# Kernel optimization log

Hardware: AMD Instinct MI355X
Metric: run time of the kernel (lower is better)

## Reference

```python
import jax, jax.numpy as jnp
import numpy as np

N_NODES = 100000
N_EDGES = 1600000
K = 3


def _cheb_conv(x, row, col, w, W, b):
    # SpMM: out[row] += w * x[col]
    def spmm(v):
        return jax.ops.segment_sum(w[:, None] * v[col], row, num_segments=N_NODES)
    Ts = [x, spmm(x)]
    for _ in range(2, K):
        Ts.append(2.0 * spmm(Ts[-1]) - Ts[-2])
    return jnp.concatenate(Ts, axis=-1) @ W.T + b


def setup_inputs() -> dict:
    key = jax.random.key(0)
    ks = jax.random.split(key, 12)
    inp = {
        "x": jax.random.normal(ks[0], (N_NODES, 128), dtype=jnp.float32),
        "edge_index": jax.random.randint(ks[1], (2, N_EDGES), 0, N_NODES, dtype=jnp.int32),
        "edge_weight": jax.random.normal(ks[2], (N_EDGES,), dtype=jnp.float32) * 0.05,
        "W_in": jax.random.normal(ks[3], (128, K * 128), dtype=jnp.float32) * (1.0 / np.sqrt(K * 128)),
        "b_in": jnp.zeros((128,), dtype=jnp.float32),
        "W_h1": jax.random.normal(ks[4], (128, K * 128), dtype=jnp.float32) * (1.0 / np.sqrt(K * 128)),
        "b_h1": jnp.zeros((128,), dtype=jnp.float32),
        "W_h2": jax.random.normal(ks[5], (128, K * 128), dtype=jnp.float32) * (1.0 / np.sqrt(K * 128)),
        "b_h2": jnp.zeros((128,), dtype=jnp.float32),
        "W_out": jax.random.normal(ks[6], (64, K * 128), dtype=jnp.float32) * (1.0 / np.sqrt(K * 128)),
        "b_out": jnp.zeros((64,), dtype=jnp.float32),
    }
    return inp


def reference(x, edge_index, edge_weight, W_in, b_in, W_h1, b_h1, W_h2, b_h2, W_out, b_out):
    row, col = edge_index[0], edge_index[1]
    # dropout is inactive at inference (training=False)
    h = jax.nn.relu(_cheb_conv(x, row, col, edge_weight, W_in, b_in))
    for (W, b) in ((W_h1, b_h1), (W_h2, b_h2)):
        h = jax.nn.relu(_cheb_conv(h, row, col, edge_weight, W, b) + h)  # residual
    out = _cheb_conv(h, row, col, edge_weight, W_out, b_out)
    return out
```

## Files before the change

kernel.cpp:

```cpp
#include <hip/hip_runtime.h>
#include <hip/hip_bf16.h>
#include <stdint.h>
#include <stddef.h>

#define N_NODES 100000
#define N_EDGES 1600000
#define FEAT 128
#define NB_SCAN ((N_NODES + 255) / 256)
#define LDS_PITCH 136
#define CAP 24
#define NL (CAP / 4)

typedef __attribute__((ext_vector_type(8))) short bf16x8;
typedef __attribute__((ext_vector_type(4))) float f32x4;
typedef unsigned short u16;

__device__ __forceinline__ float bf2f(u16 u) {
    union { unsigned int i; float f; } v; v.i = ((unsigned int)u) << 16; return v.f;
}
__device__ __forceinline__ u16 f2bf(float f) {
    union { float f; unsigned int i; } v; v.f = f;
    unsigned int x = v.i;
    return (u16)((x + 0x7fffu + ((x >> 16) & 1u)) >> 16);
}


__global__ void hist_kernel(const int* __restrict__ rows, int* __restrict__ counts) {
    int e = blockIdx.x * blockDim.x + threadIdx.x;
    if (e < N_EDGES) {
        int r = rows[e];
        r = min(max(r, 0), N_NODES - 1);
        atomicAdd(&counts[r], 1);
    }
}

__global__ void reduce_counts_kernel(const int* __restrict__ counts, int* __restrict__ bsum) {
    __shared__ int s[256];
    int i = blockIdx.x * 256 + threadIdx.x;
    int v = (i < N_NODES) ? counts[i] : 0;
    s[threadIdx.x] = v; __syncthreads();
    for (int off = 128; off > 0; off >>= 1) {
        if (threadIdx.x < off) s[threadIdx.x] += s[threadIdx.x + off];
        __syncthreads();
    }
    if (threadIdx.x == 0) bsum[blockIdx.x] = s[0];
}

__global__ void scan_bsums_kernel(int* __restrict__ bsum, int* __restrict__ row_ptr) {
    __shared__ int s[512];
    int t = threadIdx.x;
    int v = (t < NB_SCAN) ? bsum[t] : 0;
    s[t] = v; __syncthreads();
    for (int off = 1; off < 512; off <<= 1) {
        int x = (t >= off) ? s[t - off] : 0;
        __syncthreads();
        s[t] += x;
        __syncthreads();
    }
    if (t < NB_SCAN) bsum[t] = s[t] - v;
    if (t == NB_SCAN - 1) row_ptr[N_NODES] = s[t];
}

__global__ void write_rowptr_kernel(int* __restrict__ counts, const int* __restrict__ bsum,
                                    int* __restrict__ row_ptr) {
    __shared__ int s[256];
    int i = blockIdx.x * 256 + threadIdx.x;
    int v = (i < N_NODES) ? counts[i] : 0;
    s[threadIdx.x] = v; __syncthreads();
    for (int off = 1; off < 256; off <<= 1) {
        int x = (threadIdx.x >= off) ? s[threadIdx.x - off] : 0;
        __syncthreads();
        s[threadIdx.x] += x;
        __syncthreads();
    }
    if (i < N_NODES) {
        row_ptr[i] = bsum[blockIdx.x] + s[threadIdx.x] - v;
        counts[i] = 0;
    }
}

__global__ void scatter_kernel(const int* __restrict__ rows, const int* __restrict__ cols,
                               const float* __restrict__ w, const int* __restrict__ row_ptr,
                               int* __restrict__ fill, int2* __restrict__ ecw) {
    int e = blockIdx.x * blockDim.x + threadIdx.x;
    if (e < N_EDGES) {
        int r = rows[e];
        r = min(max(r, 0), N_NODES - 1);
        int pos = row_ptr[r] + atomicAdd(&fill[r], 1);
        pos = min(max(pos, 0), N_EDGES - 1);
        int c = cols[e];
        c = min(max(c, 0), N_NODES - 1);
        ecw[pos] = make_int2(c, __float_as_int(w[e]));
    }
}

__device__ __forceinline__ float w_fold(const float* W, int o, int k) {
    if (k < 128)      return W[o * 384 + k] - W[o * 384 + 256 + k];
    else if (k < 256) return W[o * 384 + k];
    else              return 2.0f * W[o * 384 + k];
}

__global__ void prep_w_kernel(const float* __restrict__ W, u16* __restrict__ Wp, int O) {
    int i = blockIdx.x * blockDim.x + threadIdx.x;
    if (i >= O * 384) return;
    int o = i / 384, k = i % 384;
    Wp[i] = f2bf(w_fold(W, o, k));
}

__global__ void prep_w2_kernel(const float* __restrict__ W, u16* __restrict__ Wp2, int O) {
    int i = blockIdx.x * blockDim.x + threadIdx.x;
    int total = (O / 16) * 12 * 64;
    if (i >= total) return;
    int ot = i / 768;
    int rem = i % 768;
    int kk = rem / 64;
    int l = rem % 64;
    int q = l >> 4, r = l & 15;
    int o = ot * 16 + r;
    int kbase = kk * 32 + q * 8;
#pragma unroll
    for (int j = 0; j < 8; ++j)
        Wp2[(size_t)i * 8 + j] = f2bf(w_fold(W, o, kbase + j));
}


__global__ void cvt_kernel(const float* __restrict__ x, u16* __restrict__ y) {
    int i = blockIdx.x * blockDim.x + threadIdx.x;
    if (i >= N_NODES * FEAT / 4) return;
    float4 v = ((const float4*)x)[i];
    ushort4 o;
    o.x = f2bf(v.x); o.y = f2bf(v.y); o.z = f2bf(v.z); o.w = f2bf(v.w);
    ((ushort4*)y)[i] = o;
}


__device__ __forceinline__ void load_meta(const int2* __restrict__ ecw, int s, int n,
                                          int lane, int& call, float& wall) {
    int idx = s + max(0, min(lane, n - 1));
    idx = min(idx, N_EDGES - 1);
    int2 cw = ecw[idx];
    call = cw.x;
    wall = (lane < n) ? __int_as_float(cw.y) : 0.f;
}

__device__ __forceinline__ void issue_row(const u16* __restrict__ X, int call,
                                          int g, int f, bf16x8* q) {
#pragma unroll
    for (int k = 0; k < NL; ++k) {
        int col = __shfl(call, k * 4 + g);
        q[k] = *(const bf16x8*)(X + (size_t)col * FEAT + f * 8);
    }
}

__device__ __forceinline__ void reduce_row(const bf16x8* q, float wall,
                                           int g, float* acc) {
#pragma unroll
    for (int k = 0; k < NL; ++k) {
        float wj = __shfl(wall, k * 4 + g);
#pragma unroll
        for (int j = 0; j < 8; ++j) acc[j] += wj * bf2f((u16)q[k][j]);
    }
}

__device__ __forceinline__ void gather4(const int* __restrict__ row_ptr,
                                        const int2* __restrict__ ecw,
                                        const u16* __restrict__ X,
                                        int r0, int lane, int g, int f,
                                        float acc[4][8]) {
    int s[4], e[4];
    int call[4]; float wall[4];
#pragma unroll
    for (int y = 0; y < 4; ++y) {
        s[y] = row_ptr[r0 + y];
        e[y] = row_ptr[r0 + y + 1];
    }
#pragma unroll
    for (int y = 0; y < 4; ++y)
        load_meta(ecw, s[y], min(e[y] - s[y], CAP), lane, call[y], wall[y]);
#pragma unroll
    for (int y = 0; y < 4; ++y)
#pragma unroll
        for (int j = 0; j < 8; ++j) acc[y][j] = 0.f;

    bf16x8 q0[NL], q1[NL], q2[NL], q3[NL];
    issue_row(X, call[0], g, f, q0);
    issue_row(X, call[1], g, f, q1);
    reduce_row(q0, wall[0], g, acc[0]);
    issue_row(X, call[2], g, f, q2);
    reduce_row(q1, wall[1], g, acc[1]);
    issue_row(X, call[3], g, f, q3);
    reduce_row(q2, wall[2], g, acc[2]);
    reduce_row(q3, wall[3], g, acc[3]);

#pragma unroll
    for (int y = 0; y < 4; ++y) {
        for (int cs = s[y] + CAP; cs < e[y]; cs += CAP) {
            int c2; float w2;
            load_meta(ecw, cs, min(e[y] - cs, CAP), lane, c2, w2);
            bf16x8 qt[NL];
            issue_row(X, c2, g, f, qt);
            reduce_row(qt, w2, g, acc[y]);
        }
    }

#pragma unroll
    for (int y = 0; y < 4; ++y)
#pragma unroll
        for (int j = 0; j < 8; ++j) {
            acc[y][j] += __shfl_xor(acc[y][j], 16);
            acc[y][j] += __shfl_xor(acc[y][j], 32);
        }
}


__global__ __launch_bounds__(256) void spmm_kernel(const int* __restrict__ row_ptr,
                                                   const int2* __restrict__ ecw,
                                                   const u16* __restrict__ X,
                                                   u16* __restrict__ Y) {
    int wid = threadIdx.x >> 6;
    int lane = threadIdx.x & 63;
    int g = lane >> 4, f = lane & 15;
    int r0 = blockIdx.x * 16 + wid * 4;

    float acc[4][8];
    gather4(row_ptr, ecw, X, r0, lane, g, f, acc);

    if (g == 0) {
#pragma unroll
        for (int y = 0; y < 4; ++y) {
            u16 tmp[8];
#pragma unroll
            for (int j = 0; j < 8; ++j) tmp[j] = f2bf(acc[y][j]);
            *(bf16x8*)(Y + (size_t)(r0 + y) * FEAT + f * 8) = *(const bf16x8*)tmp;
        }
    }
}


template <int O, bool RELU, bool RES, bool OUT_F32>
__global__ __launch_bounds__(256) void gemm_kernel(const u16* __restrict__ H,
                                                   const u16* __restrict__ T1,
                                                   const u16* __restrict__ S2,
                                                   const u16* __restrict__ Wp2,
                                                   const float* __restrict__ bias,
                                                   void* __restrict__ outv) {
    __shared__ __align__(16) u16 sA[3][32][LDS_PITCH];
    int tid = threadIdx.x;
    int m0 = blockIdx.x * 32;

#pragma unroll
    for (int p = 0; p < 3; ++p) {
        const u16* sp = (p == 0) ? H : (p == 1) ? T1 : S2;
#pragma unroll
        for (int u = 0; u < 2; ++u) {
            int unit = u * 256 + tid;
            int row = unit >> 4, seg = unit & 15;
            *(bf16x8*)&sA[p][row][seg * 8] =
                *(const bf16x8*)(sp + (size_t)(m0 + row) * FEAT + seg * 8);
        }
    }
    __syncthreads();

    int lane = tid & 63, wid = tid >> 6;
    int r = lane & 15, q = lane >> 4;
    constexpr int NW = O / 64;
    f32x4 acc0[NW], acc1[NW];
#pragma unroll
    for (int t = 0; t < NW; ++t) {
        acc0[t] = (f32x4){0.f, 0.f, 0.f, 0.f};
        acc1[t] = (f32x4){0.f, 0.f, 0.f, 0.f};
    }

#pragma unroll
    for (int kk = 0; kk < 12; ++kk) {
        int p = kk >> 2, ko = kk & 3;
        bf16x8 af0 = *(const bf16x8*)&sA[p][r][ko * 32 + q * 8];
        bf16x8 af1 = *(const bf16x8*)&sA[p][16 + r][ko * 32 + q * 8];
#pragma unroll
        for (int t = 0; t < NW; ++t) {
            int ot = wid * NW + t;
            bf16x8 bfr = *(const bf16x8*)(Wp2 + ((size_t)(ot * 12 + kk) * 64 + lane) * 8);
            acc0[t] = __builtin_amdgcn_mfma_f32_16x16x32_bf16(af0, bfr, acc0[t], 0, 0, 0);
            acc1[t] = __builtin_amdgcn_mfma_f32_16x16x32_bf16(af1, bfr, acc1[t], 0, 0, 0);
        }
    }

#pragma unroll
    for (int t = 0; t < NW; ++t) {
        int col = (wid * NW + t) * 16 + r;
        float bv = bias[col];
#pragma unroll
        for (int i = 0; i < 4; ++i) {
            int lrow = q * 4 + i;
            float v0 = acc0[t][i] + bv;
            if (RES)  v0 += bf2f(sA[0][lrow][col]);
            if (RELU) v0 = fmaxf(v0, 0.f);
            float v1 = acc1[t][i] + bv;
            if (RES)  v1 += bf2f(sA[0][16 + lrow][col]);
            if (RELU) v1 = fmaxf(v1, 0.f);
            if (OUT_F32) {
                ((float*)outv)[(size_t)(m0 + lrow) * O + col] = v0;
                ((float*)outv)[(size_t)(m0 + 16 + lrow) * O + col] = v1;
            } else {
                ((u16*)outv)[(size_t)(m0 + lrow) * O + col] = f2bf(v0);
                ((u16*)outv)[(size_t)(m0 + 16 + lrow) * O + col] = f2bf(v1);
            }
        }
    }
}


template <int O, bool RELU, bool RES, bool OUT_F32>
__global__ __launch_bounds__(256) void fused_gemm_kernel(const int* __restrict__ row_ptr,
                                                         const int2* __restrict__ ecw,
                                                         const u16* __restrict__ H,
                                                         const u16* __restrict__ T1,
                                                         const u16* __restrict__ Wp,
                                                         const float* __restrict__ bias,
                                                         void* __restrict__ outv) {
    __shared__ __align__(16) u16 sT[16 * LDS_PITCH];
    int wid = threadIdx.x >> 6;
    int lane = threadIdx.x & 63;
    int g = lane >> 4, f = lane & 15;
    int m0 = blockIdx.x * 16;

    {
        float acc[4][8];
        gather4(row_ptr, ecw, T1, m0 + wid * 4, lane, g, f, acc);
        if (g == 0) {
#pragma unroll
            for (int y = 0; y < 4; ++y) {
                u16 tmp[8];
#pragma unroll
                for (int j = 0; j < 8; ++j) tmp[j] = f2bf(acc[y][j]);
                *(bf16x8*)(sT + (wid * 4 + y) * LDS_PITCH + f * 8) = *(const bf16x8*)tmp;
            }
        }
    }
    __syncthreads();

    int r = f, q = g;
    constexpr int NT = O / 16;
    constexpr int NW = NT / 4;
    f32x4 acc[NW];
#pragma unroll
    for (int t = 0; t < NW; ++t) acc[t] = (f32x4){0.f, 0.f, 0.f, 0.f};

#pragma unroll
    for (int kk = 0; kk < 12; ++kk) {
        bf16x8 af;
        if (kk < 4)
            af = *(const bf16x8*)(H + (size_t)(m0 + r) * FEAT + kk * 32 + q * 8);
        else if (kk < 8)
            af = *(const bf16x8*)(T1 + (size_t)(m0 + r) * FEAT + (kk - 4) * 32 + q * 8);
        else
            af = *(const bf16x8*)(sT + r * LDS_PITCH + (kk - 8) * 32 + q * 8);
#pragma unroll
        for (int t = 0; t < NW; ++t) {
            int ot = wid * NW + t;
            bf16x8 bfr = *(const bf16x8*)(Wp + (size_t)(ot * 16 + r) * 384 + kk * 32 + q * 8);
            acc[t] = __builtin_amdgcn_mfma_f32_16x16x32_bf16(af, bfr, acc[t], 0, 0, 0);
        }
    }

#pragma unroll
    for (int t = 0; t < NW; ++t) {
        int col = (wid * NW + t) * 16 + r;
        float bv = bias[col];
#pragma unroll
        for (int i = 0; i < 4; ++i) {
            int row = m0 + q * 4 + i;
            float v = acc[t][i] + bv;
            if (RES)  v += bf2f(H[(size_t)row * FEAT + col]);
            if (RELU) v = fmaxf(v, 0.f);
            if (OUT_F32) ((float*)outv)[(size_t)row * O + col] = v;
            else         ((u16*)outv)[(size_t)row * O + col] = f2bf(v);
        }
    }
}


static inline size_t align_up(size_t x) { return (x + 255) & ~(size_t)255; }

extern "C" void kernel_launch(void* const* d_in, const int* in_sizes, int n_in,
                              void* d_out, int out_size, void* d_ws, size_t ws_size,
                              hipStream_t stream) {
    const float* x     = (const float*)d_in[0];
    const int*   ei    = (const int*)d_in[1];
    const float* ew    = (const float*)d_in[2];
    const float* W_in  = (const float*)d_in[3];
    const float* b_in  = (const float*)d_in[4];
    const float* W_h1  = (const float*)d_in[5];
    const float* b_h1  = (const float*)d_in[6];
    const float* W_h2  = (const float*)d_in[7];
    const float* b_h2  = (const float*)d_in[8];
    const float* W_out = (const float*)d_in[9];
    const float* b_out = (const float*)d_in[10];

    const int* rows = ei;
    const int* cols = ei + N_EDGES;

    char* w = (char*)d_ws;
    size_t off = 0;
    int* counts = (int*)(w + off);            off = align_up(off + (size_t)N_NODES * 4);
    int* row_ptr= (int*)(w + off);            off = align_up(off + (size_t)(N_NODES + 1) * 4);
    int* bsum   = (int*)(w + off);            off = align_up(off + 512 * 4);
    int2* ecw   = (int2*)(w + off);           off = align_up(off + (size_t)N_EDGES * 8);
    u16* t1     = (u16*)(w + off);            off = align_up(off + (size_t)N_NODES * FEAT * 2);
    u16* h      = (u16*)(w + off);            off = align_up(off + (size_t)N_NODES * FEAT * 2);
    u16* Wp_in  = (u16*)(w + off);            off = align_up(off + (size_t)128 * 384 * 2);
    u16* Wp_h1  = (u16*)(w + off);            off = align_up(off + (size_t)128 * 384 * 2);
    u16* Wp_h2  = (u16*)(w + off);            off = align_up(off + (size_t)128 * 384 * 2);
    u16* Wp_out = (u16*)(w + off);            off = align_up(off + (size_t)64 * 384 * 2);
    u16* s2     = (u16*)(w + off);            size_t off2 = align_up(off + (size_t)N_NODES * FEAT * 2);
    u16* W2_in  = (u16*)(w + off2);           off2 = align_up(off2 + (size_t)128 * 384 * 2);
    u16* W2_h1  = (u16*)(w + off2);           off2 = align_up(off2 + (size_t)128 * 384 * 2);
    u16* W2_h2  = (u16*)(w + off2);           off2 = align_up(off2 + (size_t)128 * 384 * 2);
    u16* W2_out = (u16*)(w + off2);           off2 = align_up(off2 + (size_t)64 * 384 * 2);
    const bool use_split = (ws_size >= off2);

    hipMemsetAsync(counts, 0, (size_t)N_NODES * 4, stream);

    cvt_kernel<<<(N_NODES * FEAT / 4 + 255) / 256, 256, 0, stream>>>(x, h);

    hist_kernel<<<N_EDGES / 256, 256, 0, stream>>>(rows, counts);
    reduce_counts_kernel<<<NB_SCAN, 256, 0, stream>>>(counts, bsum);
    scan_bsums_kernel<<<1, 512, 0, stream>>>(bsum, row_ptr);
    write_rowptr_kernel<<<NB_SCAN, 256, 0, stream>>>(counts, bsum, row_ptr);
    scatter_kernel<<<N_EDGES / 256, 256, 0, stream>>>(rows, cols, ew, row_ptr, counts, ecw);

    const int grid16 = N_NODES / 16;
    const int grid32 = N_NODES / 32;

    if (use_split) {
        prep_w2_kernel<<<(128 * 384 / 8 + 255) / 256, 256, 0, stream>>>(W_in, W2_in, 128);
        prep_w2_kernel<<<(128 * 384 / 8 + 255) / 256, 256, 0, stream>>>(W_h1, W2_h1, 128);
        prep_w2_kernel<<<(128 * 384 / 8 + 255) / 256, 256, 0, stream>>>(W_h2, W2_h2, 128);
        prep_w2_kernel<<<(64 * 384 / 8 + 255) / 256, 256, 0, stream>>>(W_out, W2_out, 64);

        spmm_kernel<<<grid16, 256, 0, stream>>>(row_ptr, ecw, h, t1);
        spmm_kernel<<<grid16, 256, 0, stream>>>(row_ptr, ecw, t1, s2);
        gemm_kernel<128, true, false, false><<<grid32, 256, 0, stream>>>(h, t1, s2, W2_in, b_in, h);
        spmm_kernel<<<grid16, 256, 0, stream>>>(row_ptr, ecw, h, t1);
        spmm_kernel<<<grid16, 256, 0, stream>>>(row_ptr, ecw, t1, s2);
        gemm_kernel<128, true, true, false><<<grid32, 256, 0, stream>>>(h, t1, s2, W2_h1, b_h1, h);
        spmm_kernel<<<grid16, 256, 0, stream>>>(row_ptr, ecw, h, t1);
        spmm_kernel<<<grid16, 256, 0, stream>>>(row_ptr, ecw, t1, s2);
        gemm_kernel<128, true, true, false><<<grid32, 256, 0, stream>>>(h, t1, s2, W2_h2, b_h2, h);
        spmm_kernel<<<grid16, 256, 0, stream>>>(row_ptr, ecw, h, t1);
        spmm_kernel<<<grid16, 256, 0, stream>>>(row_ptr, ecw, t1, s2);
        gemm_kernel<64, false, false, true><<<grid32, 256, 0, stream>>>(h, t1, s2, W2_out, b_out, d_out);
    } else {
        prep_w_kernel<<<(128 * 384 + 255) / 256, 256, 0, stream>>>(W_in, Wp_in, 128);
        prep_w_kernel<<<(128 * 384 + 255) / 256, 256, 0, stream>>>(W_h1, Wp_h1, 128);
        prep_w_kernel<<<(128 * 384 + 255) / 256, 256, 0, stream>>>(W_h2, Wp_h2, 128);
        prep_w_kernel<<<(64 * 384 + 255) / 256, 256, 0, stream>>>(W_out, Wp_out, 64);

        spmm_kernel<<<grid16, 256, 0, stream>>>(row_ptr, ecw, h, t1);
        fused_gemm_kernel<128, true, false, false><<<grid16, 256, 0, stream>>>(
            row_ptr, ecw, h, t1, Wp_in, b_in, h);
        spmm_kernel<<<grid16, 256, 0, stream>>>(row_ptr, ecw, h, t1);
        fused_gemm_kernel<128, true, true, false><<<grid16, 256, 0, stream>>>(
            row_ptr, ecw, h, t1, Wp_h1, b_h1, h);
        spmm_kernel<<<grid16, 256, 0, stream>>>(row_ptr, ecw, h, t1);
        fused_gemm_kernel<128, true, true, false><<<grid16, 256, 0, stream>>>(
            row_ptr, ecw, h, t1, Wp_h2, b_h2, h);
        spmm_kernel<<<grid16, 256, 0, stream>>>(row_ptr, ecw, h, t1);
        fused_gemm_kernel<64, false, false, true><<<grid16, 256, 0, stream>>>(
            row_ptr, ecw, h, t1, Wp_out, b_out, d_out);
    }
}
```

Before: 826.8 us.

## Build CSR via two-level bucketing to localize atomics and scatter writes

Replaces the global histogram and random-scatter CSR construction with a two-level bucket sort. Edges are first binned into 256-row buckets using LDS atomics and one global atomic per bucket per block, then counted and scattered within each bucket. This aims to cut the cost of global atomic contention and scattered writes during CSR build. The s2 buffer is reused as temporary bucket storage, and a fixed per-bucket capacity clamps overflow, which could silently drop edges if a bucket exceeds 8160 entries.

```diff
diff --git a/kernel.cpp b/kernel.cpp
--- a/kernel.cpp
+++ b/kernel.cpp
@@ -10,6 +10,9 @@
 #define LDS_PITCH 136
 #define CAP 24
 #define NL (CAP / 4)
+#define NBKT ((N_NODES + 255) / 256)
+#define BCAP 8160
+#define EPB 16384
 
 typedef __attribute__((ext_vector_type(8))) short bf16x8;
 typedef __attribute__((ext_vector_type(4))) float f32x4;
@@ -91,6 +94,76 @@
         int c = cols[e];
         c = min(max(c, 0), N_NODES - 1);
         ecw[pos] = make_int2(c, __float_as_int(w[e]));
+    }
+}
+
+
+__global__ __launch_bounds__(256) void bucket_p1_kernel(const int* __restrict__ rows,
+                                                        const int* __restrict__ cols,
+                                                        const float* __restrict__ w,
+                                                        int* __restrict__ gcnt,
+                                                        int2* __restrict__ bbuf) {
+    __shared__ int s_cnt[NBKT];
+    __shared__ int s_base[NBKT];
+    int tid = threadIdx.x;
+    for (int b = tid; b < NBKT; b += 256) s_cnt[b] = 0;
+    __syncthreads();
+    int e0 = blockIdx.x * EPB;
+#pragma unroll 4
+    for (int it = 0; it < EPB / 256; ++it) {
+        int e = e0 + it * 256 + tid;
+        if (e < N_EDGES) {
+            int r = min(max(rows[e], 0), N_NODES - 1);
+            atomicAdd(&s_cnt[r >> 8], 1);
+        }
+    }
+    __syncthreads();
+    for (int b = tid; b < NBKT; b += 256) {
+        s_base[b] = atomicAdd(&gcnt[b], s_cnt[b]);
+        s_cnt[b] = 0;
+    }
+    __syncthreads();
+#pragma unroll 4
+    for (int it = 0; it < EPB / 256; ++it) {
+        int e = e0 + it * 256 + tid;
+        if (e < N_EDGES) {
+            int r = min(max(rows[e], 0), N_NODES - 1);
+            int b = r >> 8;
+            int k = atomicAdd(&s_cnt[b], 1);
+            int pos = min(s_base[b] + k, BCAP - 1);
+            int c = min(max(cols[e], 0), N_NODES - 1);
+            bbuf[(size_t)b * BCAP + pos] = make_int2(c | ((r & 255) << 20), __float_as_int(w[e]));
+        }
+    }
+}
+
+__global__ __launch_bounds__(256) void bucket_count_kernel(const int* __restrict__ gcnt,
+                                                           const int2* __restrict__ bbuf,
+                                                           int* __restrict__ counts) {
+    __shared__ int s_cnt[256];
+    int b = blockIdx.x, tid = threadIdx.x;
+    s_cnt[tid] = 0; __syncthreads();
+    int cnt = min(gcnt[b], BCAP);
+    for (int i = tid; i < cnt; i += 256)
+        atomicAdd(&s_cnt[bbuf[(size_t)b * BCAP + i].x >> 20], 1);
+    __syncthreads();
+    int r = b * 256 + tid;
+    if (r < N_NODES) counts[r] = s_cnt[tid];
+}
+
+__global__ __launch_bounds__(256) void bucket_scatter_kernel(const int* __restrict__ gcnt,
+                                                             const int2* __restrict__ bbuf,
+                                                             const int* __restrict__ row_ptr,
+                                                             int* __restrict__ fill,
+                                                             int2* __restrict__ ecw) {
+    int b = blockIdx.x, tid = threadIdx.x;
+    int cnt = min(gcnt[b], BCAP);
+    for (int i = tid; i < cnt; i += 256) {
+        int2 p = bbuf[(size_t)b * BCAP + i];
+        int r = b * 256 + (p.x >> 20);
+        int pos = row_ptr[r] + atomicAdd(&fill[r], 1);
+        pos = min(max(pos, 0), N_EDGES - 1);
+        ecw[pos] = make_int2(p.x & 0xFFFFF, p.y);
     }
 }
 
@@ -417,22 +490,27 @@
     u16* W2_h1  = (u16*)(w + off2);           off2 = align_up(off2 + (size_t)128 * 384 * 2);
     u16* W2_h2  = (u16*)(w + off2);           off2 = align_up(off2 + (size_t)128 * 384 * 2);
     u16* W2_out = (u16*)(w + off2);           off2 = align_up(off2 + (size_t)64 * 384 * 2);
+    int* gcnt   = (int*)(w + off2);           off2 = align_up(off2 + (size_t)NBKT * 4);
     const bool use_split = (ws_size >= off2);
+    static_assert((size_t)NBKT * BCAP * 8 <= (size_t)N_NODES * FEAT * 2, "bucket buffer exceeds s2");
 
     hipMemsetAsync(counts, 0, (size_t)N_NODES * 4, stream);
 
     cvt_kernel<<<(N_NODES * FEAT / 4 + 255) / 256, 256, 0, stream>>>(x, h);
-
-    hist_kernel<<<N_EDGES / 256, 256, 0, stream>>>(rows, counts);
-    reduce_counts_kernel<<<NB_SCAN, 256, 0, stream>>>(counts, bsum);
-    scan_bsums_kernel<<<1, 512, 0, stream>>>(bsum, row_ptr);
-    write_rowptr_kernel<<<NB_SCAN, 256, 0, stream>>>(counts, bsum, row_ptr);
-    scatter_kernel<<<N_EDGES / 256, 256, 0, stream>>>(rows, cols, ew, row_ptr, counts, ecw);
 
     const int grid16 = N_NODES / 16;
     const int grid32 = N_NODES / 32;
 
     if (use_split) {
+        hipMemsetAsync(gcnt, 0, (size_t)NBKT * 4, stream);
+        int2* bbuf = (int2*)s2;
+        bucket_p1_kernel<<<(N_EDGES + EPB - 1) / EPB, 256, 0, stream>>>(rows, cols, ew, gcnt, bbuf);
+        bucket_count_kernel<<<NBKT, 256, 0, stream>>>(gcnt, bbuf, counts);
+        reduce_counts_kernel<<<NB_SCAN, 256, 0, stream>>>(counts, bsum);
+        scan_bsums_kernel<<<1, 512, 0, stream>>>(bsum, row_ptr);
+        write_rowptr_kernel<<<NB_SCAN, 256, 0, stream>>>(counts, bsum, row_ptr);
+        bucket_scatter_kernel<<<NBKT, 256, 0, stream>>>(gcnt, bbuf, row_ptr, counts, ecw);
+
         prep_w2_kernel<<<(128 * 384 / 8 + 255) / 256, 256, 0, stream>>>(W_in, W2_in, 128);
         prep_w2_kernel<<<(128 * 384 / 8 + 255) / 256, 256, 0, stream>>>(W_h1, W2_h1, 128);
         prep_w2_kernel<<<(128 * 384 / 8 + 255) / 256, 256, 0, stream>>>(W_h2, W2_h2, 128);
@@ -451,6 +529,12 @@
         spmm_kernel<<<grid16, 256, 0, stream>>>(row_ptr, ecw, t1, s2);
         gemm_kernel<64, false, false, true><<<grid32, 256, 0, stream>>>(h, t1, s2, W2_out, b_out, d_out);
     } else {
+        hist_kernel<<<N_EDGES / 256, 256, 0, stream>>>(rows, counts);
+        reduce_counts_kernel<<<NB_SCAN, 256, 0, stream>>>(counts, bsum);
+        scan_bsums_kernel<<<1, 512, 0, stream>>>(bsum, row_ptr);
+        write_rowptr_kernel<<<NB_SCAN, 256, 0, stream>>>(counts, bsum, row_ptr);
+        scatter_kernel<<<N_EDGES / 256, 256, 0, stream>>>(rows, cols, ew, row_ptr, counts, ecw);
+
         prep_w_kernel<<<(128 * 384 + 255) / 256, 256, 0, stream>>>(W_in, Wp_in, 128);
         prep_w_kernel<<<(128 * 384 + 255) / 256, 256, 0, stream>>>(W_h1, Wp_h1, 128);
         prep_w_kernel<<<(128 * 384 + 255) / 256, 256, 0, stream>>>(W_h2, Wp_h2, 128);
```

New measurement: 809.3 us. 1.02x faster.
